# Kernel optimization log

Measured on AMD Instinct MI355X. Metric: run time of the kernel, lower is better.

The kernel has to match this reference:

```python
import jax, jax.numpy as jnp
import numpy as np
from jax import lax


def setup_inputs() -> dict:
    key = jax.random.key(0)
    kx, kf = jax.random.split(key)
    x = jax.random.normal(kx, (64, 3, 224, 224), dtype=jnp.float32)
    filters = jax.random.normal(kf, (16, 3, 3, 3), dtype=jnp.float32)
    return {"x": x, "filters": filters}


def reference(x, filters):
    # Faithful math of the naive per-position matmul conv: a standard VALID
    # cross-correlation (no bias), stride=1, padding=0. Filters are OIHW.
    out = lax.conv_general_dilated(
        x, filters,
        window_strides=(1, 1),
        padding='VALID',
        dimension_numbers=('NCHW', 'OIHW', 'NCHW'),
    )
    return out  # [B, out_channels, H-k+1, W-k+1]
```

## Files before the change

kernel.cpp:

```cpp
#include <hip/hip_runtime.h>


namespace {
constexpr int B  = 64, C = 3, H = 224, W = 224;
constexpr int OC = 16, KS = 3, OH = 222, OW = 222;
constexpr int NW4   = 56;
constexpr int TOTAL = B * OH * NW4;
constexpr int BLOCK = 256;
}

__global__ __launch_bounds__(BLOCK) void conv3x3_kernel(
    const float* __restrict__ x, const float* __restrict__ flt,
    float* __restrict__ out) {
  __shared__ float flds[OC * 28];
  const int lt = threadIdx.x;
  for (int e = lt; e < OC * 27; e += BLOCK) {
    const int oc = e / 27;
    const int r  = e - oc * 27;
    flds[oc * 28 + r] = flt[e];
  }
  __syncthreads();

  const int tid = blockIdx.x * BLOCK + lt;
  if (tid >= TOTAL) return;
  const int g  = tid % NW4;
  const int t1 = tid / NW4;
  const int oh = t1 % OH;
  const int b  = t1 / OH;
  const int w0 = g * 4;
  const bool tail = (w0 + 4 > OW);
  const int  wb   = tail ? w0 : w0 + 4;

  float c8[C][KS][8];
  const float* xb = x + (size_t)b * (C * H * W);
#pragma unroll
  for (int c = 0; c < C; ++c) {
#pragma unroll
    for (int r = 0; r < KS; ++r) {
      const float* row = xb + (c * H + oh + r) * W;
      const float4 a  = *reinterpret_cast<const float4*>(row + w0);
      const float4 bb = *reinterpret_cast<const float4*>(row + wb);
      c8[c][r][0] = a.x;  c8[c][r][1] = a.y;  c8[c][r][2] = a.z;  c8[c][r][3] = a.w;
      c8[c][r][4] = bb.x; c8[c][r][5] = bb.y; c8[c][r][6] = bb.z; c8[c][r][7] = bb.w;
    }
  }

  float* outp = out + (size_t)(b * OC) * (OH * OW) + (size_t)oh * OW + w0;
#pragma unroll 1
  for (int oc = 0; oc < OC; ++oc) {
    float fr[28];
#pragma unroll
    for (int q = 0; q < 7; ++q) {
      const float4 fv = *reinterpret_cast<const float4*>(&flds[oc * 28 + q * 4]);
      fr[q * 4 + 0] = fv.x; fr[q * 4 + 1] = fv.y;
      fr[q * 4 + 2] = fv.z; fr[q * 4 + 3] = fv.w;
    }
    float a0 = 0.f, a1 = 0.f, a2 = 0.f, a3 = 0.f;
#pragma unroll
    for (int c = 0; c < C; ++c)
#pragma unroll
      for (int r = 0; r < KS; ++r)
#pragma unroll
        for (int kw = 0; kw < KS; ++kw) {
          const float wv = fr[c * 9 + r * 3 + kw];
          a0 = fmaf(wv, c8[c][r][kw + 0], a0);
          a1 = fmaf(wv, c8[c][r][kw + 1], a1);
          a2 = fmaf(wv, c8[c][r][kw + 2], a2);
          a3 = fmaf(wv, c8[c][r][kw + 3], a3);
        }
    float* op = outp + (size_t)oc * (OH * OW);
    if (!tail) {
      *reinterpret_cast<float2*>(op + 0) = make_float2(a0, a1);
      *reinterpret_cast<float2*>(op + 2) = make_float2(a2, a3);
    } else {
      op[0] = a0;
      op[1] = a1;
    }
  }
}

extern "C" void kernel_launch(void* const* d_in, const int* in_sizes, int n_in,
                              void* d_out, int out_size, void* d_ws, size_t ws_size,
                              hipStream_t stream) {
  const float* x = (const float*)d_in[0];
  const float* f = (const float*)d_in[1];
  float* o       = (float*)d_out;
  const int grid = (TOTAL + BLOCK - 1) / BLOCK;
  conv3x3_kernel<<<grid, BLOCK, 0, stream>>>(x, f, o);
}
```

Measured before the change: 259.7 us.

## Drop shared-memory filter staging, use nontemporal output stores and exact grid

Removes the LDS filter copy and its barrier, so each thread reads filter weights straight from global memory (uniform addresses, likely scalar loads) inside the oc loop. Output writes become nontemporal stores to avoid polluting cache with the large write stream. The grid now divides TOTAL exactly, so the bounds check is removed, the tail test is simplified, and launch bounds request 4 blocks per SM. The risk is added global/scalar load traffic for the filters on every oc iteration.

New measurement: 243.3 us. 6.3% less time.

```diff
diff --git a/kernel.cpp b/kernel.cpp
--- a/kernel.cpp
+++ b/kernel.cpp
@@ -7,28 +7,19 @@
 constexpr int NW4   = 56;
 constexpr int TOTAL = B * OH * NW4;
 constexpr int BLOCK = 256;
+typedef float f32x2 __attribute__((ext_vector_type(2)));
 }
 
-__global__ __launch_bounds__(BLOCK) void conv3x3_kernel(
+__global__ __launch_bounds__(BLOCK, 4) void conv3x3_kernel(
     const float* __restrict__ x, const float* __restrict__ flt,
     float* __restrict__ out) {
-  __shared__ float flds[OC * 28];
-  const int lt = threadIdx.x;
-  for (int e = lt; e < OC * 27; e += BLOCK) {
-    const int oc = e / 27;
-    const int r  = e - oc * 27;
-    flds[oc * 28 + r] = flt[e];
-  }
-  __syncthreads();
-
-  const int tid = blockIdx.x * BLOCK + lt;
-  if (tid >= TOTAL) return;
+  const int tid = blockIdx.x * BLOCK + threadIdx.x;
   const int g  = tid % NW4;
   const int t1 = tid / NW4;
   const int oh = t1 % OH;
   const int b  = t1 / OH;
   const int w0 = g * 4;
-  const bool tail = (w0 + 4 > OW);
+  const bool tail = (g == NW4 - 1);
   const int  wb   = tail ? w0 : w0 + 4;
 
   float c8[C][KS][8];
@@ -48,13 +39,10 @@
   float* outp = out + (size_t)(b * OC) * (OH * OW) + (size_t)oh * OW + w0;
 #pragma unroll 1
   for (int oc = 0; oc < OC; ++oc) {
-    float fr[28];
+    float fv[27];
 #pragma unroll
-    for (int q = 0; q < 7; ++q) {
-      const float4 fv = *reinterpret_cast<const float4*>(&flds[oc * 28 + q * 4]);
-      fr[q * 4 + 0] = fv.x; fr[q * 4 + 1] = fv.y;
-      fr[q * 4 + 2] = fv.z; fr[q * 4 + 3] = fv.w;
-    }
+    for (int k = 0; k < 27; ++k) fv[k] = flt[oc * 27 + k];
+
     float a0 = 0.f, a1 = 0.f, a2 = 0.f, a3 = 0.f;
 #pragma unroll
     for (int c = 0; c < C; ++c)
@@ -62,19 +50,22 @@
       for (int r = 0; r < KS; ++r)
 #pragma unroll
         for (int kw = 0; kw < KS; ++kw) {
-          const float wv = fr[c * 9 + r * 3 + kw];
+          const float wv = fv[c * 9 + r * 3 + kw];
           a0 = fmaf(wv, c8[c][r][kw + 0], a0);
           a1 = fmaf(wv, c8[c][r][kw + 1], a1);
           a2 = fmaf(wv, c8[c][r][kw + 2], a2);
           a3 = fmaf(wv, c8[c][r][kw + 3], a3);
         }
+
     float* op = outp + (size_t)oc * (OH * OW);
     if (!tail) {
-      *reinterpret_cast<float2*>(op + 0) = make_float2(a0, a1);
-      *reinterpret_cast<float2*>(op + 2) = make_float2(a2, a3);
+      f32x2 v01; v01.x = a0; v01.y = a1;
+      f32x2 v23; v23.x = a2; v23.y = a3;
+      __builtin_nontemporal_store(v01, reinterpret_cast<f32x2*>(op));
+      __builtin_nontemporal_store(v23, reinterpret_cast<f32x2*>(op) + 1);
     } else {
-      op[0] = a0;
-      op[1] = a1;
+      __builtin_nontemporal_store(a0, op + 0);
+      __builtin_nontemporal_store(a1, op + 1);
     }
   }
 }
@@ -85,6 +76,6 @@
   const float* x = (const float*)d_in[0];
   const float* f = (const float*)d_in[1];
   float* o       = (float*)d_out;
-  const int grid = (TOTAL + BLOCK - 1) / BLOCK;
+  const int grid = TOTAL / BLOCK;
   conv3x3_kernel<<<grid, BLOCK, 0, stream>>>(x, f, o);
 }
```
